# Kernel optimization log

Hardware: AMD Instinct MI355X
Metric: run time of the kernel (lower is better)

The kernel has to match this reference:

```python
import jax, jax.numpy as jnp
import numpy as np

EPS = 1e-5  # torch BatchNorm1d default eps

# BinActive: sign forward, straight-through estimator backward (grad clipped where |x|>1)
@jax.custom_vjp
def bin_active(x):
    return jnp.sign(x)

def _ba_fwd(x):
    return jnp.sign(x), x

def _ba_bwd(x, g):
    return (g * (jnp.abs(x) <= 1.0).astype(g.dtype),)

bin_active.defvjp(_ba_fwd, _ba_bwd)

# XNOR-style weight binarization: sign(W) * mean(|W|) per output column, STE backward
@jax.custom_vjp
def bin_weight(w):
    alpha = jnp.mean(jnp.abs(w), axis=0, keepdims=True)  # [1, out]
    return jnp.sign(w) * alpha

def _bw_fwd(w):
    alpha = jnp.mean(jnp.abs(w), axis=0, keepdims=True)
    return jnp.sign(w) * alpha, w

def _bw_bwd(w, g):
    return (g * (jnp.abs(w) <= 1.0).astype(g.dtype),)

bin_weight.defvjp(_bw_fwd, _bw_bwd)


def setup_inputs() -> dict:
    key = jax.random.key(0)
    ks = jax.random.split(key, 8)
    N, E, IN, H, OUT = 100000, 1600000, 256, 128, 40
    x = jax.random.normal(ks[0], (N, IN), dtype=jnp.float32)
    edge_index = jax.random.randint(ks[1], (2, E), 0, N, dtype=jnp.int64)
    W0 = jax.random.normal(ks[2], (IN, H), dtype=jnp.float32) * (2.0 / IN) ** 0.5
    b0 = jnp.zeros((H,), dtype=jnp.float32)
    W1 = jax.random.normal(ks[3], (H, H), dtype=jnp.float32) * (2.0 / H) ** 0.5
    b1 = jnp.zeros((H,), dtype=jnp.float32)
    W2 = jax.random.normal(ks[4], (H, OUT), dtype=jnp.float32) * (2.0 / H) ** 0.5
    b2 = jnp.zeros((OUT,), dtype=jnp.float32)
    return {"x": x, "edge_index": edge_index, "W0": W0, "b0": b0,
            "W1": W1, "b1": b1, "W2": W2, "b2": b2}


def reference(x, edge_index, W0, b0, W1, b1, W2, b2):
    n = x.shape[0]
    loop = jnp.arange(n, dtype=edge_index.dtype)
    src = jnp.concatenate([edge_index[0], loop])  # add self loops (GCN norm)
    dst = jnp.concatenate([edge_index[1], loop])
    deg = jax.ops.segment_sum(jnp.ones_like(src, dtype=x.dtype), dst, num_segments=n)
    dinv = jnp.where(deg > 0, deg ** -0.5, 0.0)
    norm = (dinv[src] * dinv[dst])[:, None]  # [E+N, 1]

    # BatchNorm1d(affine=False), training-mode batch statistics (biased var)
    mu = jnp.mean(x, axis=0)
    var = jnp.var(x, axis=0)
    h = (x - mu) * jax.lax.rsqrt(var + EPS)

    for W, b in ((W0, b0), (W1, b1), (W2, b2)):
        h = bin_active(h)                       # sign binarize (dropout skipped: eval)
        h = h @ bin_weight(W)                   # binary-weight linear
        h = jax.ops.segment_sum(h[src] * norm, dst, num_segments=n) + b  # D^-1/2 (A+I) D^-1/2 agg
    return jax.nn.log_softmax(h, axis=1)
```

## Files before the change

### kernel.cpp

```cpp
#include <hip/hip_runtime.h>
#include <math.h>

#define IN_DIM 256
#define HD 128
#define OUT_DIM 40
#define S2_STRIDE 64
#define NB_CS 512

__global__ __launch_bounds__(256) void k_init(int* deg, float* muacc, int N) {
    int i = blockIdx.x * 256 + threadIdx.x;
    if (i < N) deg[i] = 1;
    if (blockIdx.x == 0 && threadIdx.x < 256) muacc[threadIdx.x] = 0.f;
}

__global__ __launch_bounds__(256) void k_fuse1(const float* __restrict__ x, int N,
                                               float* __restrict__ muacc,
                                               const int* __restrict__ ei, int E, int* deg,
                                               int* __restrict__ rank, int ebl,
                                               const float* __restrict__ W0,
                                               const float* __restrict__ W1,
                                               const float* __restrict__ W2,
                                               unsigned long long* W0p,
                                               unsigned long long* W1p,
                                               unsigned long long* W2p,
                                               float* aS0, float* aS1, float* aS2) {
    __shared__ float lds[256];
    int b = blockIdx.x, tid = threadIdx.x;
    if (b < NB_CS) {
        size_t F4 = (size_t)N * (IN_DIM / 4);
        size_t stride = (size_t)NB_CS * 256;
        float a0 = 0.f, a1 = 0.f, a2 = 0.f, a3 = 0.f;
        const float4* x4 = (const float4*)x;
        for (size_t i = (size_t)b * 256 + tid; i < F4; i += stride) {
            float4 v = x4[i];
            a0 += v.x; a1 += v.y; a2 += v.z; a3 += v.w;
        }
        lds[tid] = 0.f;
        __syncthreads();
        int c0 = (tid * 4) & 255;
        atomicAdd(&lds[c0], a0);
        atomicAdd(&lds[c0 + 1], a1);
        atomicAdd(&lds[c0 + 2], a2);
        atomicAdd(&lds[c0 + 3], a3);
        __syncthreads();
        atomicAdd(&muacc[tid], lds[tid]);
    } else if (b < NB_CS + ebl) {
        int e = (b - NB_CS) * 256 + tid;
        if (e < E) {
            int old = atomicAdd(&deg[ei[E + e]], 1);
            rank[e] = old - 1;
        }
    } else {
        int b2 = b - NB_CS - ebl;
        int lane = tid & 63, w = tid >> 6;
        if (b2 < 32) {
            int j = b2 * 4 + w;
            float asum = 0.f;
            unsigned long long words[4];
            #pragma unroll
            for (int q = 0; q < 4; ++q) {
                float v = W0[(size_t)(4 * lane + q) * HD + j];
                asum += fabsf(v);
                words[q] = __ballot(v < 0.f);
            }
            #pragma unroll
            for (int off = 32; off; off >>= 1) asum += __shfl_xor(asum, off);
            if (lane == 0) {
                aS0[j] = 2.f * asum / 256.f;
                #pragma unroll
                for (int q = 0; q < 4; ++q) W0p[j * 4 + q] = words[q];
            }
        } else if (b2 < 64) {
            int j = (b2 - 32) * 4 + w;
            int fl = lane & 15, kk = lane >> 4;
            float asum = 0.f;
            unsigned long long words[2];
            #pragma unroll
            for (int q = 0; q < 2; ++q) {
                float v = W1[(size_t)(fl * 8 + 4 * q + kk) * HD + j];
                asum += fabsf(v);
                words[q] = __ballot(v < 0.f);
            }
            #pragma unroll
            for (int off = 32; off; off >>= 1) asum += __shfl_xor(asum, off);
            if (lane == 0) {
                aS1[j] = 2.f * asum / 128.f;
                W1p[j * 2 + 0] = words[0];
                W1p[j * 2 + 1] = words[1];
            }
        } else {
            int j = (b2 - 64) * 4 + w;
            int fl = lane & 15, kk = lane >> 4;
            if (j < OUT_DIM) {
                float asum = 0.f;
                unsigned long long words[2];
                #pragma unroll
                for (int q = 0; q < 2; ++q) {
                    float v = W2[(size_t)(fl * 8 + 4 * q + kk) * OUT_DIM + j];
                    asum += fabsf(v);
                    words[q] = __ballot(v < 0.f);
                }
                #pragma unroll
                for (int off = 32; off; off >>= 1) asum += __shfl_xor(asum, off);
                if (lane == 0) {
                    aS2[j] = 2.f * asum / 128.f;
                    W2p[j * 2 + 0] = words[0];
                    W2p[j * 2 + 1] = words[1];
                }
            }
        }
    }
}

__global__ __launch_bounds__(256) void k_bp(const int* __restrict__ deg, int N, int* bp) {
    __shared__ int sm[256];
    int i = blockIdx.x * 256 + threadIdx.x;
    sm[threadIdx.x] = (i < N) ? (deg[i] - 1) : 0;
    __syncthreads();
    for (int off = 128; off; off >>= 1) {
        if (threadIdx.x < off) sm[threadIdx.x] += sm[threadIdx.x + off];
        __syncthreads();
    }
    if (threadIdx.x == 0) bp[blockIdx.x] = sm[0];
}

__global__ __launch_bounds__(512) void k_scanbp(const int* __restrict__ bp, int NB, int* bps) {
    __shared__ int sm[512];
    int t = threadIdx.x;
    int v = (t < NB) ? bp[t] : 0;
    sm[t] = v;
    __syncthreads();
    for (int off = 1; off < 512; off <<= 1) {
        int add = (t >= off) ? sm[t - off] : 0;
        __syncthreads();
        sm[t] += add;
        __syncthreads();
    }
    if (t < NB) bps[t] = sm[t] - v;
}

__global__ __launch_bounds__(256) void k_rowptr(const int* __restrict__ deg,
                                                const int* __restrict__ bps, int N, int E,
                                                int* row_ptr, float* dinv) {
    __shared__ int wsum[4];
    int t = threadIdx.x, lane = t & 63, w = t >> 6;
    int i = blockIdx.x * 256 + t;
    int c = (i < N) ? (deg[i] - 1) : 0;
    int v = c;
    #pragma unroll
    for (int off = 1; off < 64; off <<= 1) {
        int n = __shfl_up(v, off);
        if (lane >= off) v += n;
    }
    if (lane == 63) wsum[w] = v;
    __syncthreads();
    int wo = 0;
    for (int k = 0; k < w; ++k) wo += wsum[k];
    int excl = bps[blockIdx.x] + wo + v - c;
    if (i < N) {
        row_ptr[i] = excl;
        dinv[i] = (float)(1.0 / sqrt((double)deg[i]));
    }
    if (blockIdx.x == 0 && t == 0) row_ptr[N] = E;
}

__global__ __launch_bounds__(256) void k_fuse2(const int* __restrict__ ei, int E,
                                               const float* __restrict__ dinv,
                                               const int* __restrict__ rowp,
                                               const int* __restrict__ rank,
                                               long long* __restrict__ cs, int nbScat,
                                               const float* __restrict__ x,
                                               const float* __restrict__ muacc, float inv_n,
                                               const unsigned long long* __restrict__ W0p,
                                               unsigned char* __restrict__ S0, int N) {
    __shared__ unsigned long long w0s[128 * 4];
    int b = blockIdx.x, tid = threadIdx.x;
    if (b < nbScat) {
        int e = b * 256 + tid;
        if (e >= E) return;
        int s = ei[e];
        int d = ei[E + e];
        int pos = rowp[d] + rank[e];
        float nrm = dinv[s] * dinv[d];
        long long v = (long long)(unsigned int)s |
                      ((long long)(unsigned int)__float_as_int(nrm) << 32);
        __builtin_nontemporal_store(v, &cs[pos]);
    } else {
        w0s[tid] = W0p[tid];
        w0s[tid + 256] = W0p[tid + 256];
        __syncthreads();
        int lane = tid & 63;
        int row = (b - nbScat) * 4 + (tid >> 6);
        if (row >= N) return;
        float4 xv = ((const float4*)(x + (size_t)row * IN_DIM))[lane];
        float4 ms = ((const float4*)muacc)[lane];
        unsigned long long xw[4];
        xw[0] = __ballot(xv.x < ms.x * inv_n);
        xw[1] = __ballot(xv.y < ms.y * inv_n);
        xw[2] = __ballot(xv.z < ms.z * inv_n);
        xw[3] = __ballot(xv.w < ms.w * inv_n);
        unsigned int pack = 0;
        #pragma unroll
        for (int t2 = 0; t2 < 2; ++t2) {
            int j = 2 * lane + t2;
            const unsigned long long* wc = &w0s[j * 4];
            int dd = __popcll(xw[0] ^ wc[0]) + __popcll(xw[1] ^ wc[1]) +
                     __popcll(xw[2] ^ wc[2]) + __popcll(xw[3] ^ wc[3]);
            int S = IN_DIM - 2 * dd;
            int s8 = S >> 1;
            if (s8 > 127) s8 = 127;
            pack |= ((unsigned int)(s8 + 128) & 0xffu) << (8 * t2);
        }
        *(unsigned short*)(S0 + (size_t)row * HD + 2 * lane) = (unsigned short)pack;
    }
}

template <int OUTC>
__global__ __launch_bounds__(256) void k_agg_mm(const unsigned char* __restrict__ Sin,
                                                const int* __restrict__ row_ptr,
                                                const long long* __restrict__ cs,
                                                const float* __restrict__ dinv,
                                                const float* __restrict__ alphaS,
                                                const float* __restrict__ bias,
                                                const unsigned long long* __restrict__ Wnp,
                                                unsigned char* __restrict__ Sout, int N) {
    __shared__ unsigned long long wsm[OUTC * 2];
    int tid = threadIdx.x;
    for (int i = tid; i < OUTC * 2; i += 256) wsm[i] = Wnp[i];
    __syncthreads();
    int lane = tid & 63;
    int d = blockIdx.x * 4 + (tid >> 6);
    if (d >= N) return;
    int sub = lane >> 4;
    int fl  = lane & 15;
    float acc[8];
    #pragma unroll
    for (int k = 0; k < 8; ++k) acc[k] = 0.f;
    if (sub == 0) {
        float dv = dinv[d];
        float nrm = dv * dv;
        unsigned long long r = *(const unsigned long long*)(Sin + (size_t)d * HD + fl * 8);
        unsigned int lo = (unsigned int)r, hi = (unsigned int)(r >> 32);
        #pragma unroll
        for (int k = 0; k < 4; ++k) {
            acc[k]     = fmaf(nrm, (float)((lo >> (8 * k)) & 0xffu) - 128.f, acc[k]);
            acc[k + 4] = fmaf(nrm, (float)((hi >> (8 * k)) & 0xffu) - 128.f, acc[k + 4]);
        }
    }
    int e0 = row_ptr[d], e1 = row_ptr[d + 1];
    int e = e0 + sub;
    for (; e + 4 < e1; e += 8) {
        long long pa = cs[e];
        long long pb = cs[e + 4];
        int sa = (int)(unsigned int)pa;
        int sb = (int)(unsigned int)pb;
        unsigned long long ra = *(const unsigned long long*)(Sin + (size_t)sa * HD + fl * 8);
        unsigned long long rb = *(const unsigned long long*)(Sin + (size_t)sb * HD + fl * 8);
        float na = __int_as_float((int)(pa >> 32));
        float nb = __int_as_float((int)(pb >> 32));
        unsigned int la = (unsigned int)ra, ha = (unsigned int)(ra >> 32);
        unsigned int lb = (unsigned int)rb, hb = (unsigned int)(rb >> 32);
        #pragma unroll
        for (int k = 0; k < 4; ++k) {
            acc[k]     = fmaf(na, (float)((la >> (8 * k)) & 0xffu) - 128.f, acc[k]);
            acc[k + 4] = fmaf(na, (float)((ha >> (8 * k)) & 0xffu) - 128.f, acc[k + 4]);
            acc[k]     = fmaf(nb, (float)((lb >> (8 * k)) & 0xffu) - 128.f, acc[k]);
            acc[k + 4] = fmaf(nb, (float)((hb >> (8 * k)) & 0xffu) - 128.f, acc[k + 4]);
        }
    }
    if (e < e1) {
        long long p = cs[e];
        int s = (int)(unsigned int)p;
        float nrm = __int_as_float((int)(p >> 32));
        unsigned long long r = *(const unsigned long long*)(Sin + (size_t)s * HD + fl * 8);
        unsigned int lo = (unsigned int)r, hi = (unsigned int)(r >> 32);
        #pragma unroll
        for (int k = 0; k < 4; ++k) {
            acc[k]     = fmaf(nrm, (float)((lo >> (8 * k)) & 0xffu) - 128.f, acc[k]);
            acc[k + 4] = fmaf(nrm, (float)((hi >> (8 * k)) & 0xffu) - 128.f, acc[k + 4]);
        }
    }
    #pragma unroll
    for (int k = 0; k < 8; ++k) {
        acc[k] += __shfl_xor(acc[k], 16);
        acc[k] += __shfl_xor(acc[k], 32);
    }
    unsigned int m8 = 0;
    #pragma unroll
    for (int k = 0; k < 8; ++k) {
        int f = fl * 8 + k;
        float v = alphaS[f] * acc[k] + bias[f];
        if (v < 0.f) m8 |= (1u << k);
    }
    unsigned long long x0 = 0, x1 = 0;
    #pragma unroll
    for (int k = 0; k < 4; ++k) {
        unsigned long long bk = __ballot((m8 >> k) & 1u);
        x0 |= (bk & 0xffffULL) << (16 * k);
    }
    #pragma unroll
    for (int k = 4; k < 8; ++k) {
        unsigned long long bk = __ballot((m8 >> k) & 1u);
        x1 |= (bk & 0xffffULL) << (16 * (k - 4));
    }
    if (OUTC == 128) {
        unsigned int pack = 0;
        #pragma unroll
        for (int t2 = 0; t2 < 2; ++t2) {
            int j = 2 * lane + t2;
            int dd = __popcll(x0 ^ wsm[j * 2]) + __popcll(x1 ^ wsm[j * 2 + 1]);
            int S = HD - 2 * dd;
            pack |= ((unsigned int)((S >> 1) + 128) & 0xffu) << (8 * t2);
        }
        *(unsigned short*)(Sout + (size_t)d * HD + 2 * lane) = (unsigned short)pack;
    } else {
        int p8 = 128;
        if (lane < OUTC) {
            int dd = __popcll(x0 ^ wsm[lane * 2]) + __popcll(x1 ^ wsm[lane * 2 + 1]);
            p8 = ((HD - 2 * dd) >> 1) + 128;
        }
        Sout[(size_t)d * S2_STRIDE + lane] = (unsigned char)p8;
    }
}

__global__ __launch_bounds__(256) void k_agg_out(const unsigned char* __restrict__ S2,
                                                 const int* __restrict__ row_ptr,
                                                 const long long* __restrict__ cs,
                                                 const float* __restrict__ dinv,
                                                 const float* __restrict__ alphaS2,
                                                 const float* __restrict__ b2,
                                                 float* __restrict__ out, int N) {
    int tid = threadIdx.x, lane = tid & 63;
    int d = blockIdx.x * 4 + (tid >> 6);
    if (d >= N) return;
    int sub = lane >> 4;
    int fl  = lane & 15;
    float acc[4] = {0.f, 0.f, 0.f, 0.f};
    if (sub == 0) {
        float dv = dinv[d];
        float nrm = dv * dv;
        unsigned int r4 = *(const unsigned int*)(S2 + (size_t)d * S2_STRIDE + fl * 4);
        #pragma unroll
        for (int k = 0; k < 4; ++k)
            acc[k] = fmaf(nrm, (float)((r4 >> (8 * k)) & 0xffu) - 128.f, acc[k]);
    }
    int e0 = row_ptr[d], e1 = row_ptr[d + 1];
    int e = e0 + sub;
    for (; e + 4 < e1; e += 8) {
        long long pa = cs[e];
        long long pb = cs[e + 4];
        int sa = (int)(unsigned int)pa;
        int sb = (int)(unsigned int)pb;
        unsigned int ra = *(const unsigned int*)(S2 + (size_t)sa * S2_STRIDE + fl * 4);
        unsigned int rb = *(const unsigned int*)(S2 + (size_t)sb * S2_STRIDE + fl * 4);
        float na = __int_as_float((int)(pa >> 32));
        float nb = __int_as_float((int)(pb >> 32));
        #pragma unroll
        for (int k = 0; k < 4; ++k) {
            acc[k] = fmaf(na, (float)((ra >> (8 * k)) & 0xffu) - 128.f, acc[k]);
            acc[k] = fmaf(nb, (float)((rb >> (8 * k)) & 0xffu) - 128.f, acc[k]);
        }
    }
    if (e < e1) {
        long long p = cs[e];
        int s = (int)(unsigned int)p;
        float nrm = __int_as_float((int)(p >> 32));
        unsigned int r4 = *(const unsigned int*)(S2 + (size_t)s * S2_STRIDE + fl * 4);
        #pragma unroll
        for (int k = 0; k < 4; ++k)
            acc[k] = fmaf(nrm, (float)((r4 >> (8 * k)) & 0xffu) - 128.f, acc[k]);
    }
    #pragma unroll
    for (int k = 0; k < 4; ++k) {
        acc[k] += __shfl_xor(acc[k], 16);
        acc[k] += __shfl_xor(acc[k], 32);
    }
    float h[4];
    float mymax = -INFINITY;
    #pragma unroll
    for (int k = 0; k < 4; ++k) {
        int f = fl * 4 + k;
        h[k] = (f < OUT_DIM) ? (alphaS2[f] * acc[k] + b2[f]) : -INFINITY;
        mymax = fmaxf(mymax, h[k]);
    }
    #pragma unroll
    for (int off = 1; off < 16; off <<= 1) mymax = fmaxf(mymax, __shfl_xor(mymax, off));
    float s4 = 0.f;
    #pragma unroll
    for (int k = 0; k < 4; ++k) {
        if (fl * 4 + k < OUT_DIM) s4 += expf(h[k] - mymax);
    }
    #pragma unroll
    for (int off = 1; off < 16; off <<= 1) s4 += __shfl_xor(s4, off);
    float lse = mymax + logf(s4);
    if (sub == 0 && fl < OUT_DIM / 4) {
        float4 o;
        o.x = h[0] - lse; o.y = h[1] - lse; o.z = h[2] - lse; o.w = h[3] - lse;
        *(float4*)(out + (size_t)d * OUT_DIM + fl * 4) = o;
    }
}

extern "C" void kernel_launch(void* const* d_in, const int* in_sizes, int n_in,
                              void* d_out, int out_size, void* d_ws, size_t ws_size,
                              hipStream_t stream) {
    const float* x  = (const float*)d_in[0];
    const int*   ei = (const int*)d_in[1];
    const float* W0 = (const float*)d_in[2];
    const float* b0 = (const float*)d_in[3];
    const float* W1 = (const float*)d_in[4];
    const float* b1 = (const float*)d_in[5];
    const float* W2 = (const float*)d_in[6];
    const float* b2 = (const float*)d_in[7];
    float* out = (float*)d_out;

    int N = in_sizes[0] / IN_DIM;
    int E = in_sizes[1] / 2;

    char* ws = (char*)d_ws;
    size_t off = 0;
    auto alloc = [&](size_t bytes) -> void* {
        off = (off + 255) & ~(size_t)255;
        void* p = (void*)(ws + off);
        off += bytes;
        return p;
    };
    float* muacc  = (float*)alloc(256 * 4);
    int*   deg    = (int*)alloc((size_t)N * 4);
    float* dinv   = (float*)alloc((size_t)N * 4);
    int*   rowp   = (int*)alloc(((size_t)N + 1) * 4);
    int*   bp     = (int*)alloc(512 * 4);
    int*   bps    = (int*)alloc(512 * 4);
    int*   rank   = (int*)alloc((size_t)E * 4);
    long long* cs = (long long*)alloc((size_t)E * 8);
    unsigned char* S0 = (unsigned char*)alloc((size_t)N * HD);
    unsigned char* S1 = (unsigned char*)alloc((size_t)N * HD);
    unsigned char* S2 = (unsigned char*)alloc((size_t)N * S2_STRIDE);
    unsigned long long* W0p = (unsigned long long*)alloc(128 * 4 * 8);
    unsigned long long* W1p = (unsigned long long*)alloc(128 * 2 * 8);
    unsigned long long* W2p = (unsigned long long*)alloc(40 * 2 * 8);
    float* aS0 = (float*)alloc(128 * 4);
    float* aS1 = (float*)alloc(128 * 4);
    float* aS2 = (float*)alloc(40 * 4);

    int nb256 = (N + 255) / 256;
    int ebl = (E + 255) / 256;
    float inv_n = 1.0f / (float)N;

    k_init<<<dim3(nb256), dim3(256), 0, stream>>>(deg, muacc, N);
    k_fuse1<<<dim3(NB_CS + ebl + 74), dim3(256), 0, stream>>>(
        x, N, muacc, ei, E, deg, rank, ebl, W0, W1, W2, W0p, W1p, W2p, aS0, aS1, aS2);
    k_bp<<<dim3(nb256), dim3(256), 0, stream>>>(deg, N, bp);
    k_scanbp<<<dim3(1), dim3(512), 0, stream>>>(bp, nb256, bps);
    k_rowptr<<<dim3(nb256), dim3(256), 0, stream>>>(deg, bps, N, E, rowp, dinv);

    int nb4 = (N + 3) / 4;
    k_fuse2<<<dim3(ebl + nb4), dim3(256), 0, stream>>>(
        ei, E, dinv, rowp, rank, cs, ebl, x, muacc, inv_n, W0p, S0, N);
    k_agg_mm<128><<<dim3(nb4), dim3(256), 0, stream>>>(S0, rowp, cs, dinv, aS0, b0, W1p, S1, N);
    k_agg_mm<40><<<dim3(nb4), dim3(256), 0, stream>>>(S1, rowp, cs, dinv, aS1, b1, W2p, S2, N);
    k_agg_out<<<dim3(nb4), dim3(256), 0, stream>>>(S2, rowp, cs, dinv, aS2, b2, out, N);
    (void)out_size; (void)ws_size; (void)n_in;
}
```

Baseline: 512.6 us.

## Shrink CSR edges to 4-byte indices, recompute norm from dinv, chunk edge loops

The CSR edge array now stores only the 32-bit source index, not a packed index+norm pair, so the scatter write and every aggregation pass moves half as many edge bytes. The per-edge norm is rebuilt in the aggregation kernels as dinv[src]*dinv[dst], which adds a random 4-byte gather per edge. Each 16-lane subgroup now walks a contiguous chunk of a node's edge list, unrolled by four for more loads in flight. Separately, the column-mean pass gets more blocks and a two-way unrolled loop, and the weight-packing blocks are moved ahead of the degree-counting blocks in the launch order.

After: 554.1 us. 1.08x slower.

```diff
diff --git a/kernel.cpp b/kernel.cpp
--- a/kernel.cpp
+++ b/kernel.cpp
@@ -5,7 +5,8 @@
 #define HD 128
 #define OUT_DIM 40
 #define S2_STRIDE 64
-#define NB_CS 512
+#define NB_CS 2048
+#define NB_WP 74
 
 __global__ __launch_bounds__(256) void k_init(int* deg, float* muacc, int N) {
     int i = blockIdx.x * 256 + threadIdx.x;
@@ -16,7 +17,7 @@
 __global__ __launch_bounds__(256) void k_fuse1(const float* __restrict__ x, int N,
                                                float* __restrict__ muacc,
                                                const int* __restrict__ ei, int E, int* deg,
-                                               int* __restrict__ rank, int ebl,
+                                               int* __restrict__ rank,
                                                const float* __restrict__ W0,
                                                const float* __restrict__ W1,
                                                const float* __restrict__ W2,
@@ -31,7 +32,13 @@
         size_t stride = (size_t)NB_CS * 256;
         float a0 = 0.f, a1 = 0.f, a2 = 0.f, a3 = 0.f;
         const float4* x4 = (const float4*)x;
-        for (size_t i = (size_t)b * 256 + tid; i < F4; i += stride) {
+        size_t i = (size_t)b * 256 + tid;
+        for (; i + stride < F4; i += 2 * stride) {
+            float4 v = x4[i];
+            float4 w = x4[i + stride];
+            a0 += v.x + w.x; a1 += v.y + w.y; a2 += v.z + w.z; a3 += v.w + w.w;
+        }
+        if (i < F4) {
             float4 v = x4[i];
             a0 += v.x; a1 += v.y; a2 += v.z; a3 += v.w;
         }
@@ -44,14 +51,8 @@
         atomicAdd(&lds[c0 + 3], a3);
         __syncthreads();
         atomicAdd(&muacc[tid], lds[tid]);
-    } else if (b < NB_CS + ebl) {
-        int e = (b - NB_CS) * 256 + tid;
-        if (e < E) {
-            int old = atomicAdd(&deg[ei[E + e]], 1);
-            rank[e] = old - 1;
-        }
-    } else {
-        int b2 = b - NB_CS - ebl;
+    } else if (b < NB_CS + NB_WP) {
+        int b2 = b - NB_CS;
         int lane = tid & 63, w = tid >> 6;
         if (b2 < 32) {
             int j = b2 * 4 + w;
@@ -109,6 +110,12 @@
                 }
             }
         }
+    } else {
+        int e = (b - NB_CS - NB_WP) * 256 + tid;
+        if (e < E) {
+            int old = atomicAdd(&deg[ei[E + e]], 1);
+            rank[e] = old - 1;
+        }
     }
 }
 
@@ -165,10 +172,9 @@
 }
 
 __global__ __launch_bounds__(256) void k_fuse2(const int* __restrict__ ei, int E,
-                                               const float* __restrict__ dinv,
                                                const int* __restrict__ rowp,
                                                const int* __restrict__ rank,
-                                               long long* __restrict__ cs, int nbScat,
+                                               int* __restrict__ cs, int nbScat,
                                                const float* __restrict__ x,
                                                const float* __restrict__ muacc, float inv_n,
                                                const unsigned long long* __restrict__ W0p,
@@ -181,10 +187,7 @@
         int s = ei[e];
         int d = ei[E + e];
         int pos = rowp[d] + rank[e];
-        float nrm = dinv[s] * dinv[d];
-        long long v = (long long)(unsigned int)s |
-                      ((long long)(unsigned int)__float_as_int(nrm) << 32);
-        __builtin_nontemporal_store(v, &cs[pos]);
+        __builtin_nontemporal_store(s, &cs[pos]);
     } else {
         w0s[tid] = W0p[tid];
         w0s[tid + 256] = W0p[tid + 256];
@@ -218,7 +221,7 @@
 template <int OUTC>
 __global__ __launch_bounds__(256) void k_agg_mm(const unsigned char* __restrict__ Sin,
                                                 const int* __restrict__ row_ptr,
-                                                const long long* __restrict__ cs,
+                                                const int* __restrict__ cs,
                                                 const float* __restrict__ dinv,
                                                 const float* __restrict__ alphaS,
                                                 const float* __restrict__ bias,
@@ -236,9 +239,9 @@
     float acc[8];
     #pragma unroll
     for (int k = 0; k < 8; ++k) acc[k] = 0.f;
+    float dvd = dinv[d];
     if (sub == 0) {
-        float dv = dinv[d];
-        float nrm = dv * dv;
+        float nrm = dvd * dvd;
         unsigned long long r = *(const unsigned long long*)(Sin + (size_t)d * HD + fl * 8);
         unsigned int lo = (unsigned int)r, hi = (unsigned int)(r >> 32);
         #pragma unroll
@@ -248,31 +251,39 @@
         }
     }
     int e0 = row_ptr[d], e1 = row_ptr[d + 1];
-    int e = e0 + sub;
-    for (; e + 4 < e1; e += 8) {
-        long long pa = cs[e];
-        long long pb = cs[e + 4];
-        int sa = (int)(unsigned int)pa;
-        int sb = (int)(unsigned int)pb;
+    int len = e1 - e0;
+    int chunk = (len + 3) >> 2;
+    int ce0 = e0 + sub * chunk;
+    int ce1 = min(ce0 + chunk, e1);
+    int e = ce0;
+    for (; e + 3 < ce1; e += 4) {
+        int sa = cs[e], sb = cs[e + 1], sc = cs[e + 2], sd = cs[e + 3];
         unsigned long long ra = *(const unsigned long long*)(Sin + (size_t)sa * HD + fl * 8);
         unsigned long long rb = *(const unsigned long long*)(Sin + (size_t)sb * HD + fl * 8);
-        float na = __int_as_float((int)(pa >> 32));
-        float nb = __int_as_float((int)(pb >> 32));
+        unsigned long long rc = *(const unsigned long long*)(Sin + (size_t)sc * HD + fl * 8);
+        unsigned long long rd = *(const unsigned long long*)(Sin + (size_t)sd * HD + fl * 8);
+        float na = dinv[sa] * dvd, nb = dinv[sb] * dvd;
+        float nc = dinv[sc] * dvd, nd = dinv[sd] * dvd;
         unsigned int la = (unsigned int)ra, ha = (unsigned int)(ra >> 32);
         unsigned int lb = (unsigned int)rb, hb = (unsigned int)(rb >> 32);
+        unsigned int lc = (unsigned int)rc, hc = (unsigned int)(rc >> 32);
+        unsigned int ld = (unsigned int)rd, hd2 = (unsigned int)(rd >> 32);
         #pragma unroll
         for (int k = 0; k < 4; ++k) {
             acc[k]     = fmaf(na, (float)((la >> (8 * k)) & 0xffu) - 128.f, acc[k]);
             acc[k + 4] = fmaf(na, (float)((ha >> (8 * k)) & 0xffu) - 128.f, acc[k + 4]);
             acc[k]     = fmaf(nb, (float)((lb >> (8 * k)) & 0xffu) - 128.f, acc[k]);
             acc[k + 4] = fmaf(nb, (float)((hb >> (8 * k)) & 0xffu) - 128.f, acc[k + 4]);
-        }
-    }
-    if (e < e1) {
-        long long p = cs[e];
-        int s = (int)(unsigned int)p;
-        float nrm = __int_as_float((int)(p >> 32));
+            acc[k]     = fmaf(nc, (float)((lc >> (8 * k)) & 0xffu) - 128.f, acc[k]);
+            acc[k + 4] = fmaf(nc, (float)((hc >> (8 * k)) & 0xffu) - 128.f, acc[k + 4]);
+            acc[k]     = fmaf(nd, (float)((ld >> (8 * k)) & 0xffu) - 128.f, acc[k]);
+            acc[k + 4] = fmaf(nd, (float)((hd2 >> (8 * k)) & 0xffu) - 128.f, acc[k + 4]);
+        }
+    }
+    for (; e < ce1; ++e) {
+        int s = cs[e];
         unsigned long long r = *(const unsigned long long*)(Sin + (size_t)s * HD + fl * 8);
+        float nrm = dinv[s] * dvd;
         unsigned int lo = (unsigned int)r, hi = (unsigned int)(r >> 32);
         #pragma unroll
         for (int k = 0; k < 4; ++k) {
@@ -325,7 +336,7 @@
 
 __global__ __launch_bounds__(256) void k_agg_out(const unsigned char* __restrict__ S2,
                                                  const int* __restrict__ row_ptr,
-                                                 const long long* __restrict__ cs,
+                                                 const int* __restrict__ cs,
                                                  const float* __restrict__ dinv,
                                                  const float* __restrict__ alphaS2,
                                                  const float* __restrict__ b2,
@@ -336,36 +347,40 @@
     int sub = lane >> 4;
     int fl  = lane & 15;
     float acc[4] = {0.f, 0.f, 0.f, 0.f};
+    float dvd = dinv[d];
     if (sub == 0) {
-        float dv = dinv[d];
-        float nrm = dv * dv;
+        float nrm = dvd * dvd;
         unsigned int r4 = *(const unsigned int*)(S2 + (size_t)d * S2_STRIDE + fl * 4);
         #pragma unroll
         for (int k = 0; k < 4; ++k)
             acc[k] = fmaf(nrm, (float)((r4 >> (8 * k)) & 0xffu) - 128.f, acc[k]);
     }
     int e0 = row_ptr[d], e1 = row_ptr[d + 1];
-    int e = e0 + sub;
-    for (; e + 4 < e1; e += 8) {
-        long long pa = cs[e];
-        long long pb = cs[e + 4];
-        int sa = (int)(unsigned int)pa;
-        int sb = (int)(unsigned int)pb;
+    int len = e1 - e0;
+    int chunk = (len + 3) >> 2;
+    int ce0 = e0 + sub * chunk;
+    int ce1 = min(ce0 + chunk, e1);
+    int e = ce0;
+    for (; e + 3 < ce1; e += 4) {
+        int sa = cs[e], sb = cs[e + 1], sc = cs[e + 2], sd = cs[e + 3];
         unsigned int ra = *(const unsigned int*)(S2 + (size_t)sa * S2_STRIDE + fl * 4);
         unsigned int rb = *(const unsigned int*)(S2 + (size_t)sb * S2_STRIDE + fl * 4);
-        float na = __int_as_float((int)(pa >> 32));
-        float nb = __int_as_float((int)(pb >> 32));
+        unsigned int rc = *(const unsigned int*)(S2 + (size_t)sc * S2_STRIDE + fl * 4);
+        unsigned int rd = *(const unsigned int*)(S2 + (size_t)sd * S2_STRIDE + fl * 4);
+        float na = dinv[sa] * dvd, nb = dinv[sb] * dvd;
+        float nc = dinv[sc] * dvd, nd = dinv[sd] * dvd;
         #pragma unroll
         for (int k = 0; k < 4; ++k) {
             acc[k] = fmaf(na, (float)((ra >> (8 * k)) & 0xffu) - 128.f, acc[k]);
             acc[k] = fmaf(nb, (float)((rb >> (8 * k)) & 0xffu) - 128.f, acc[k]);
-        }
-    }
-    if (e < e1) {
-        long long p = cs[e];
-        int s = (int)(unsigned int)p;
-        float nrm = __int_as_float((int)(p >> 32));
+            acc[k] = fmaf(nc, (float)((rc >> (8 * k)) & 0xffu) - 128.f, acc[k]);
+            acc[k] = fmaf(nd, (float)((rd >> (8 * k)) & 0xffu) - 128.f, acc[k]);
+        }
+    }
+    for (; e < ce1; ++e) {
+        int s = cs[e];
         unsigned int r4 = *(const unsigned int*)(S2 + (size_t)s * S2_STRIDE + fl * 4);
+        float nrm = dinv[s] * dvd;
         #pragma unroll
         for (int k = 0; k < 4; ++k)
             acc[k] = fmaf(nrm, (float)((r4 >> (8 * k)) & 0xffu) - 128.f, acc[k]);
@@ -431,7 +446,7 @@
     int*   bp     = (int*)alloc(512 * 4);
     int*   bps    = (int*)alloc(512 * 4);
     int*   rank   = (int*)alloc((size_t)E * 4);
-    long long* cs = (long long*)alloc((size_t)E * 8);
+    int*   cs     = (int*)alloc((size_t)E * 4);
     unsigned char* S0 = (unsigned char*)alloc((size_t)N * HD);
     unsigned char* S1 = (unsigned char*)alloc((size_t)N * HD);
     unsigned char* S2 = (unsigned char*)alloc((size_t)N * S2_STRIDE);
@@ -447,15 +462,15 @@
     float inv_n = 1.0f / (float)N;
 
     k_init<<<dim3(nb256), dim3(256), 0, stream>>>(deg, muacc, N);
-    k_fuse1<<<dim3(NB_CS + ebl + 74), dim3(256), 0, stream>>>(
-        x, N, muacc, ei, E, deg, rank, ebl, W0, W1, W2, W0p, W1p, W2p, aS0, aS1, aS2);
+    k_fuse1<<<dim3(NB_CS + NB_WP + ebl), dim3(256), 0, stream>>>(
+        x, N, muacc, ei, E, deg, rank, W0, W1, W2, W0p, W1p, W2p, aS0, aS1, aS2);
     k_bp<<<dim3(nb256), dim3(256), 0, stream>>>(deg, N, bp);
     k_scanbp<<<dim3(1), dim3(512), 0, stream>>>(bp, nb256, bps);
     k_rowptr<<<dim3(nb256), dim3(256), 0, stream>>>(deg, bps, N, E, rowp, dinv);
 
     int nb4 = (N + 3) / 4;
     k_fuse2<<<dim3(ebl + nb4), dim3(256), 0, stream>>>(
-        ei, E, dinv, rowp, rank, cs, ebl, x, muacc, inv_n, W0p, S0, N);
+        ei, E, rowp, rank, cs, ebl, x, muacc, inv_n, W0p, S0, N);
     k_agg_mm<128><<<dim3(nb4), dim3(256), 0, stream>>>(S0, rowp, cs, dinv, aS0, b0, W1p, S1, N);
     k_agg_mm<40><<<dim3(nb4), dim3(256), 0, stream>>>(S1, rowp, cs, dinv, aS1, b1, W2p, S2, N);
     k_agg_out<<<dim3(nb4), dim3(256), 0, stream>>>(S2, rowp, cs, dinv, aS2, b2, out, N);
```
